# Optimization experiments

Hardware: AMD Instinct MI355X
Metric: run time of the kernel (lower is better)

The kernel has to match this reference:

```python
import jax, jax.numpy as jnp
import numpy as np
import itertools

N_SET = 4        # number of elements in the input set (input.size(-2))
IN_F = 2048      # in_features
OUT_F = 2048     # out_features
BOT = 512        # bottleneck_dim
B = 512          # batch size
NUM_NODES = 391
EMB_DIM = 300

# All nonempty subsets of range(N_SET), ordered by scale then lexicographic,
# exactly matching the torch loop over scales / itertools.combinations.
SUBSETS = [c for s in range(1, N_SET + 1) for c in itertools.combinations(range(N_SET), s)]

def _incl_matrix():
    # M[i, j] = 1 if SUBSETS[j] is a subset of SUBSETS[i].
    # This reproduces the dict-based scatter-sum: the aggregated output for rset
    # is the sum of raw Relation outputs over all nonempty k \subseteq rset.
    masks = [sum(1 << i for i in c) for c in SUBSETS]
    n = len(masks)
    M = np.zeros((n, n), dtype=np.float32)
    for i, mi in enumerate(masks):
        for j, mj in enumerate(masks):
            if (mj & mi) == mj:
                M[i, j] = 1.0
    return M

INCL = _incl_matrix()  # [15, 15]

def setup_inputs():
    key = jax.random.key(0)
    ks = jax.random.split(key, 16)
    inp = {"x": jax.random.normal(ks[0], (B, N_SET, IN_F), dtype=jnp.float32)}
    ki = 1
    for s in range(1, N_SET + 1):
        fan = s * IN_F
        inp[f"w1_s{s}"] = jax.random.normal(ks[ki], (BOT, fan), dtype=jnp.float32) / np.float32(np.sqrt(fan)); ki += 1
        inp[f"b1_s{s}"] = jnp.zeros((BOT,), dtype=jnp.float32)
        inp[f"w2_s{s}"] = jax.random.normal(ks[ki], (OUT_F, BOT), dtype=jnp.float32) / np.float32(np.sqrt(BOT)); ki += 1
        inp[f"b2_s{s}"] = jnp.zeros((OUT_F,), dtype=jnp.float32)
    inp["w_emb"] = jax.random.normal(ks[ki], (EMB_DIM, OUT_F), dtype=jnp.float32) / np.float32(np.sqrt(OUT_F)); ki += 1
    inp["b_emb"] = jnp.zeros((EMB_DIM,), dtype=jnp.float32)
    inp["w_node"] = jax.random.normal(ks[ki], (NUM_NODES, OUT_F), dtype=jnp.float32) / np.float32(np.sqrt(OUT_F)); ki += 1
    inp["b_node"] = jnp.zeros((NUM_NODES,), dtype=jnp.float32)
    return inp

def _base_forward(x, ws):
    # Batched per-scale Relation MLPs over all C(4,s) subsets at once.
    raws = []
    for s in range(1, N_SET + 1):
        idx = np.array(list(itertools.combinations(range(N_SET), s)))  # [C, s]
        g = x[:, idx, :]                                  # [B, C, s, F] gather
        h = g.reshape(g.shape[0], g.shape[1], s * IN_F)   # concat along subset
        w1, b1, w2, b2 = ws[s - 1]
        h = jax.nn.relu(h)
        h = jax.nn.relu(jnp.einsum('bcf,of->bco', h, w1) + b1)
        raws.append(jnp.einsum('bcd,od->bco', h, w2) + b2)  # [B, C, OUT_F]
    raw = jnp.concatenate(raws, axis=1)  # [B, 15, OUT_F]
    # Subset-inclusion scatter-sum, expressed as a dense 15x15 contraction.
    return jnp.einsum('ij,bjf->bif', jnp.asarray(INCL), raw)

def reference(x, w1_s1, b1_s1, w2_s1, b2_s1, w1_s2, b1_s2, w2_s2, b2_s2,
              w1_s3, b1_s3, w2_s3, b2_s3, w1_s4, b1_s4, w2_s4, b2_s4,
              w_emb, b_emb, w_node, b_node):
    ws = [(w1_s1, b1_s1, w2_s1, b2_s1), (w1_s2, b1_s2, w2_s2, b2_s2),
          (w1_s3, b1_s3, w2_s3, b2_s3), (w1_s4, b1_s4, w2_s4, b2_s4)]
    feats = _base_forward(x, ws)                              # [B, 15, OUT_F]
    embeddings = jnp.einsum('bnf,ef->bne', feats, w_emb) + b_emb  # [B, 15, 300]
    node_out = jnp.einsum('bnf,vf->bnv', feats, w_node) + b_node  # [B, 15, 391]
    return embeddings, jnp.swapaxes(node_out, -2, -1)             # [B, 391, 15]
```

## Files before the change

### kernel.cpp

```cpp
#include <hip/hip_runtime.h>
#include <stdint.h>

using bf16x8 = __attribute__((ext_vector_type(8))) short;
using f32x4  = __attribute__((ext_vector_type(4))) float;

#define DEVINL __device__ __forceinline__

DEVINL unsigned short f2bf(float f) {
  union { float f; unsigned u; } v; v.f = f;
  unsigned u = v.u;
  return (unsigned short)((u + 0x7FFFu + ((u >> 16) & 1u)) >> 16);
}
DEVINL float bf2f(unsigned short h) {
  union { unsigned u; float f; } v; v.u = ((unsigned)h) << 16;
  return v.f;
}

DEVINL void gload_lds16(const void* g, void* l) {
  __builtin_amdgcn_global_load_lds(
      (const __attribute__((address_space(1))) void*)g,
      (__attribute__((address_space(3))) void*)l, 16, 0, 0);
}

template<int OUT_BF16, int HAS_BIAS>
DEVINL void gemm_core(const unsigned short* __restrict__ A,
                      const unsigned short* __restrict__ B,
                      void* __restrict__ C,
                      const float* __restrict__ bias,
                      int K, int Cld, int arow0, int brow0, int crow0, int ccol0)
{
  __shared__ __align__(16) unsigned short As[3][256 * 64];
  __shared__ __align__(16) unsigned short Bs[3][128 * 64];

  const int t    = threadIdx.x;
  const int wave = t >> 6;
  const int lane = t & 63;
  const int wr   = (wave >> 1) << 6;
  const int wc   = (wave & 1) << 6;
  const int lrow = lane & 15;
  const int kg   = lane >> 4;

  f32x4 acc[4][4];
#pragma unroll
  for (int r = 0; r < 4; ++r)
#pragma unroll
    for (int q = 0; q < 4; ++q) acc[r][q] = (f32x4){0.f, 0.f, 0.f, 0.f};

  const int srow = t >> 3;
  const int scol = (((t & 7) ^ (srow & 7)) << 3);
  const unsigned short* aSrc = A + (size_t)(arow0 + srow) * K + scol;
  const unsigned short* bSrc = B + (size_t)(brow0 + srow) * K + scol;

  auto STAGE = [&](int slot, int kt) {
    const int k0 = kt << 6;
    char* aD = (char*)As[slot] + wave * 1024;
    char* bD = (char*)Bs[slot] + wave * 1024;
#pragma unroll
    for (int p = 0; p < 4; ++p)
      gload_lds16(aSrc + (size_t)(p * 64) * K + k0, aD + p * 8192);
#pragma unroll
    for (int p = 0; p < 2; ++p)
      gload_lds16(bSrc + (size_t)(p * 64) * K + k0, bD + p * 8192);
  };

  const int nt = K >> 6;
  STAGE(0, 0);
  STAGE(1, 1);

  const int rs = lrow & 7;
  const int cA0 = ((kg + 0) ^ rs) << 3;
  const int cA1 = ((kg + 4) ^ rs) << 3;

  int sl = 0;
  for (int kt = 0; kt < nt; ++kt) {
    const unsigned short* Ab = As[sl];
    const unsigned short* Bb = Bs[sl];
    if (kt + 2 < nt) {
      int s2 = sl + 2; if (s2 >= 3) s2 -= 3;
      STAGE(s2, kt + 2);
      asm volatile("s_waitcnt vmcnt(12)" ::: "memory");
    } else if (kt + 1 < nt) {
      asm volatile("s_waitcnt vmcnt(6)" ::: "memory");
    } else {
      asm volatile("s_waitcnt vmcnt(0)" ::: "memory");
    }
    __builtin_amdgcn_s_barrier();

    bf16x8 a0[4], b0[4], a1[4], b1[4];
#pragma unroll
    for (int r = 0; r < 4; ++r)
      a0[r] = *(const bf16x8*)&Ab[(wr + r * 16 + lrow) * 64 + cA0];
#pragma unroll
    for (int q = 0; q < 4; ++q)
      b0[q] = *(const bf16x8*)&Bb[(wc + q * 16 + lrow) * 64 + cA0];
    __builtin_amdgcn_s_setprio(1);
#pragma unroll
    for (int r = 0; r < 2; ++r)
#pragma unroll
      for (int q = 0; q < 4; ++q)
        acc[r][q] = __builtin_amdgcn_mfma_f32_16x16x32_bf16(a0[r], b0[q], acc[r][q], 0, 0, 0);
    __builtin_amdgcn_s_setprio(0);
    __builtin_amdgcn_s_barrier();
#pragma unroll
    for (int r = 0; r < 4; ++r)
      a1[r] = *(const bf16x8*)&Ab[(wr + r * 16 + lrow) * 64 + cA1];
#pragma unroll
    for (int q = 0; q < 4; ++q)
      b1[q] = *(const bf16x8*)&Bb[(wc + q * 16 + lrow) * 64 + cA1];
    __builtin_amdgcn_s_setprio(1);
#pragma unroll
    for (int r = 2; r < 4; ++r)
#pragma unroll
      for (int q = 0; q < 4; ++q)
        acc[r][q] = __builtin_amdgcn_mfma_f32_16x16x32_bf16(a0[r], b0[q], acc[r][q], 0, 0, 0);
    __builtin_amdgcn_s_setprio(0);
    __builtin_amdgcn_s_barrier();
    __builtin_amdgcn_s_setprio(1);
#pragma unroll
    for (int r = 0; r < 2; ++r)
#pragma unroll
      for (int q = 0; q < 4; ++q)
        acc[r][q] = __builtin_amdgcn_mfma_f32_16x16x32_bf16(a1[r], b1[q], acc[r][q], 0, 0, 0);
    __builtin_amdgcn_s_setprio(0);
    __builtin_amdgcn_s_barrier();
    __builtin_amdgcn_s_setprio(1);
#pragma unroll
    for (int r = 2; r < 4; ++r)
#pragma unroll
      for (int q = 0; q < 4; ++q)
        acc[r][q] = __builtin_amdgcn_mfma_f32_16x16x32_bf16(a1[r], b1[q], acc[r][q], 0, 0, 0);
    __builtin_amdgcn_s_setprio(0);
    __builtin_amdgcn_s_barrier();
    ++sl; if (sl == 3) sl = 0;
  }

#pragma unroll
  for (int r = 0; r < 4; ++r) {
#pragma unroll
    for (int q = 0; q < 4; ++q) {
      const int col = ccol0 + wc + q * 16 + lrow;
      const float bv = HAS_BIAS ? bias[col] : 0.f;
#pragma unroll
      for (int v = 0; v < 4; ++v) {
        const int row = crow0 + wr + r * 16 + (kg << 2) + v;
        const float val = acc[r][q][v] + bv;
        if (OUT_BF16)
          ((unsigned short*)C)[(size_t)row * Cld + col] = f2bf(val);
        else
          ((float*)C)[(size_t)row * Cld + col] = val;
      }
    }
  }
}

__global__ __launch_bounds__(512) void mega1_k(const unsigned short* __restrict__ xrb,
                                               const unsigned short* __restrict__ w1cat,
                                               const unsigned short* __restrict__ wen,
                                               const unsigned short* __restrict__ w2t,
                                               unsigned short* __restrict__ H0p,
                                               unsigned short* __restrict__ W2EN) {
  const int bid = blockIdx.x;
  if (bid < 160) {
    const int p = bid >> 3, q = bid & 7;
    const int rt = q >> 2, ct = q & 3;
    const int MM[20] = {0,1,2,3, 0,1,2, 1,2,3, 0,1, 1,2, 2,3, 0,1,2,3};
    const int JJ[20] = {0,0,0,0, 1,1,1, 2,2,2, 3,3, 4,4, 5,5, 6,7,8,9};
    gemm_core<1, 0>(xrb, w1cat, H0p, nullptr, 2048, 512,
                    MM[p] * 512 + rt * 256, JJ[p] * 512 + ct * 128,
                    p * 512 + rt * 256, ct * 128);
  } else {
    const int b2 = bid - 160;
    const int s = b2 / 12, r = b2 % 12;
    const int rt = r >> 2, ct = r & 3;
    gemm_core<1, 0>(wen, w2t, W2EN, nullptr, 2048, 512,
                    rt * 256, s * 512 + ct * 128,
                    s * 768 + rt * 256, ct * 128);
  }
}

__global__ __launch_bounds__(512) void gemmF_k(const unsigned short* __restrict__ h1,
                                               const unsigned short* __restrict__ W2EN,
                                               const float* __restrict__ ENb,
                                               float* __restrict__ EN0) {
  const int y = blockIdx.y;
  const int c = y >> 1;
  const int s = (c < 4) ? 1 : (c < 10) ? 2 : (c < 14) ? 3 : 4;
  gemm_core<0, 1>(h1, W2EN, EN0, ENb + (size_t)(s - 1) * 768, 512, 768,
                  y * 256, (s - 1) * 768 + blockIdx.x * 128,
                  y * 256, blockIdx.x * 128);
}

__global__ __launch_bounds__(256) void prep_all_k(const float* __restrict__ x,
                                                  const float* w11, const float* w12,
                                                  const float* w13, const float* w14,
                                                  const float* w21, const float* w22,
                                                  const float* w23, const float* w24,
                                                  const float* __restrict__ wemb,
                                                  const float* __restrict__ wnode,
                                                  const float* b21, const float* b22,
                                                  const float* b23, const float* b24,
                                                  unsigned short* __restrict__ xrb,
                                                  unsigned short* __restrict__ w1cat,
                                                  unsigned short* __restrict__ w2t,
                                                  unsigned short* __restrict__ wen,
                                                  float* __restrict__ ENb) {
  __shared__ float lds[64][65];
  __shared__ float red[4][4];
  const int bid = blockIdx.x;
  if (bid < 10240) {
    const int tid = bid * 256 + threadIdx.x;
    const int r = tid >> 9;
    const int k = (tid & 511) << 2;
    const int j = r >> 9, o = r & 511;
    const float* src; int s, tt;
    if (j == 0)      { src = w11; s = 1; tt = 0; }
    else if (j < 3)  { src = w12; s = 2; tt = j - 1; }
    else if (j < 6)  { src = w13; s = 3; tt = j - 3; }
    else             { src = w14; s = 4; tt = j - 6; }
    const float4 vv = *(const float4*)(src + (size_t)o * (s * 2048) + tt * 2048 + k);
    ushort4 ov;
    ov.x = f2bf(vv.x); ov.y = f2bf(vv.y); ov.z = f2bf(vv.z); ov.w = f2bf(vv.w);
    *(ushort4*)(w1cat + (size_t)r * 2048 + k) = ov;
  } else if (bid < 14336) {
    const int tid = (bid - 10240) * 256 + threadIdx.x;
    const int r = tid >> 9;
    const int k = (tid & 511) << 2;
    const int m = r >> 9, b = r & 511;
    const float4 vv = *(const float4*)(x + ((size_t)(b * 4 + m)) * 2048 + k);
    ushort4 o;
    o.x = f2bf(fmaxf(vv.x, 0.f)); o.y = f2bf(fmaxf(vv.y, 0.f));
    o.z = f2bf(fmaxf(vv.z, 0.f)); o.w = f2bf(fmaxf(vv.w, 0.f));
    *(ushort4*)(xrb + (size_t)r * 2048 + k) = o;
  } else if (bid < 15360) {
    const int idx = bid - 14336;
    const int s = idx >> 8, rem = idx & 255;
    const int rt = rem >> 3, ct = rem & 7;
    const float* src = (s == 0) ? w21 : (s == 1) ? w22 : (s == 2) ? w23 : w24;
    const int tr = threadIdx.x >> 4;
    const int tc = (threadIdx.x & 15) << 2;
#pragma unroll
    for (int i = 0; i < 4; ++i) {
      const float4 v = *(const float4*)(src + (size_t)(rt * 64 + tr + 16 * i) * 512 + ct * 64 + tc);
      lds[tr + 16 * i][tc + 0] = v.x; lds[tr + 16 * i][tc + 1] = v.y;
      lds[tr + 16 * i][tc + 2] = v.z; lds[tr + 16 * i][tc + 3] = v.w;
    }
    __syncthreads();
#pragma unroll
    for (int i = 0; i < 4; ++i) {
      ushort4 ov;
      ov.x = f2bf(lds[tc + 0][tr + 16 * i]); ov.y = f2bf(lds[tc + 1][tr + 16 * i]);
      ov.z = f2bf(lds[tc + 2][tr + 16 * i]); ov.w = f2bf(lds[tc + 3][tr + 16 * i]);
      *(ushort4*)(w2t + ((size_t)s * 512 + ct * 64 + tr + 16 * i) * 2048 + rt * 64 + tc) = ov;
    }
  } else if (bid < 16896) {
    const int tid = (bid - 15360) * 256 + threadIdx.x;
    const int r = tid >> 9;
    const int k = (tid & 511) << 2;
    float4 vv = make_float4(0.f, 0.f, 0.f, 0.f);
    if (r < 300)       vv = *(const float4*)(wemb + (size_t)r * 2048 + k);
    else if (r < 691)  vv = *(const float4*)(wnode + (size_t)(r - 300) * 2048 + k);
    ushort4 ov;
    ov.x = f2bf(vv.x); ov.y = f2bf(vv.y); ov.z = f2bf(vv.z); ov.w = f2bf(vv.w);
    *(ushort4*)(wen + (size_t)r * 2048 + k) = ov;
  } else {
    const int e = bid - 16896;
    const int t8 = threadIdx.x << 3;
    float a0 = 0.f, a1 = 0.f, a2 = 0.f, a3 = 0.f;
    if (e < 691) {
      const float* row = (e < 300) ? (wemb + (size_t)e * 2048)
                                   : (wnode + (size_t)(e - 300) * 2048);
      const float4 r0 = *(const float4*)(row + t8);
      const float4 r1 = *(const float4*)(row + t8 + 4);
      const float4 c10 = *(const float4*)(b21 + t8), c11 = *(const float4*)(b21 + t8 + 4);
      const float4 c20 = *(const float4*)(b22 + t8), c21 = *(const float4*)(b22 + t8 + 4);
      const float4 c30 = *(const float4*)(b23 + t8), c31 = *(const float4*)(b23 + t8 + 4);
      const float4 c40 = *(const float4*)(b24 + t8), c41 = *(const float4*)(b24 + t8 + 4);
      a0 = r0.x*c10.x + r0.y*c10.y + r0.z*c10.z + r0.w*c10.w
         + r1.x*c11.x + r1.y*c11.y + r1.z*c11.z + r1.w*c11.w;
      a1 = r0.x*c20.x + r0.y*c20.y + r0.z*c20.z + r0.w*c20.w
         + r1.x*c21.x + r1.y*c21.y + r1.z*c21.z + r1.w*c21.w;
      a2 = r0.x*c30.x + r0.y*c30.y + r0.z*c30.z + r0.w*c30.w
         + r1.x*c31.x + r1.y*c31.y + r1.z*c31.z + r1.w*c31.w;
      a3 = r0.x*c40.x + r0.y*c40.y + r0.z*c40.z + r0.w*c40.w
         + r1.x*c41.x + r1.y*c41.y + r1.z*c41.z + r1.w*c41.w;
    }
#pragma unroll
    for (int off = 32; off; off >>= 1) {
      a0 += __shfl_down(a0, off); a1 += __shfl_down(a1, off);
      a2 += __shfl_down(a2, off); a3 += __shfl_down(a3, off);
    }
    const int wv = threadIdx.x >> 6;
    if ((threadIdx.x & 63) == 0) {
      red[wv][0] = a0; red[wv][1] = a1; red[wv][2] = a2; red[wv][3] = a3;
    }
    __syncthreads();
    if (threadIdx.x < 4) {
      const float v = red[0][threadIdx.x] + red[1][threadIdx.x] +
                      red[2][threadIdx.x] + red[3][threadIdx.x];
      ENb[(size_t)threadIdx.x * 768 + e] = (e < 691) ? v : 0.f;
    }
  }
}

__global__ __launch_bounds__(128) void combine1_k(const unsigned short* __restrict__ H0p,
                                                  unsigned short* __restrict__ h1,
                                                  const float* __restrict__ b11,
                                                  const float* __restrict__ b12,
                                                  const float* __restrict__ b13,
                                                  const float* __restrict__ b14) {
  const int cb = blockIdx.x;
  const int c = cb >> 9, b = cb & 511;
  const int s = (c < 4) ? 1 : (c < 10) ? 2 : (c < 14) ? 3 : 4;
  const unsigned char P[15][4] = {
    {0,0,0,0},{1,0,0,0},{2,0,0,0},{3,0,0,0},
    {4,7,0,0},{4,8,0,0},{4,9,0,0},{5,8,0,0},{5,9,0,0},{6,9,0,0},
    {10,12,14,0},{10,12,15,0},{10,13,15,0},{11,13,15,0},
    {16,17,18,19}};
  const float* b1 = (s == 1) ? b11 : (s == 2) ? b12 : (s == 3) ? b13 : b14;
  const int o = threadIdx.x << 2;
  float4 a = *(const float4*)(b1 + o);
  for (int t = 0; t < s; ++t) {
    const int p = P[c][t];
    const ushort4 hv = *(const ushort4*)(H0p + ((size_t)(p * 512 + b)) * 512 + o);
    a.x += bf2f(hv.x); a.y += bf2f(hv.y); a.z += bf2f(hv.z); a.w += bf2f(hv.w);
  }
  ushort4 ov;
  ov.x = f2bf(fmaxf(a.x, 0.f)); ov.y = f2bf(fmaxf(a.y, 0.f));
  ov.z = f2bf(fmaxf(a.z, 0.f)); ov.w = f2bf(fmaxf(a.w, 0.f));
  *(ushort4*)(h1 + (size_t)cb * 512 + o) = ov;
}

__global__ __launch_bounds__(256) void combine2_k(const float* __restrict__ EN0,
                                                  const float* __restrict__ b_emb,
                                                  const float* __restrict__ b_node,
                                                  float* __restrict__ out0,
                                                  float* __restrict__ out1) {
  const int b   = blockIdx.x;
  const int col = blockIdx.y * 256 + threadIdx.x;
  if (col >= 691) return;
  float vals[15];
#pragma unroll
  for (int j = 0; j < 15; ++j)
    vals[j] = EN0[((size_t)(j * 512 + b)) * 768 + col];
  const int MSK[15] = {1,2,4,8,3,5,9,6,10,12,7,11,13,14,15};
  if (col < 300) {
    const float be = b_emb[col];
#pragma unroll
    for (int i = 0; i < 15; ++i) {
      float sum = be;
#pragma unroll
      for (int j = 0; j < 15; ++j)
        if ((MSK[j] & MSK[i]) == MSK[j]) sum += vals[j];
      out0[((size_t)b * 15 + i) * 300 + col] = sum;
    }
  } else {
    const int v = col - 300;
    const float bn = b_node[v];
#pragma unroll
    for (int i = 0; i < 15; ++i) {
      float sum = bn;
#pragma unroll
      for (int j = 0; j < 15; ++j)
        if ((MSK[j] & MSK[i]) == MSK[j]) sum += vals[j];
      out1[((size_t)b * 391 + v) * 15 + i] = sum;
    }
  }
}

extern "C" void kernel_launch(void* const* d_in, const int* in_sizes, int n_in,
                              void* d_out, int out_size, void* d_ws, size_t ws_size,
                              hipStream_t stream) {
  const float* x     = (const float*)d_in[0];
  const float* w11   = (const float*)d_in[1];
  const float* b11   = (const float*)d_in[2];
  const float* w21   = (const float*)d_in[3];
  const float* b21   = (const float*)d_in[4];
  const float* w12   = (const float*)d_in[5];
  const float* b12   = (const float*)d_in[6];
  const float* w22   = (const float*)d_in[7];
  const float* b22   = (const float*)d_in[8];
  const float* w13   = (const float*)d_in[9];
  const float* b13   = (const float*)d_in[10];
  const float* w23   = (const float*)d_in[11];
  const float* b23   = (const float*)d_in[12];
  const float* w14   = (const float*)d_in[13];
  const float* b14   = (const float*)d_in[14];
  const float* w24   = (const float*)d_in[15];
  const float* b24   = (const float*)d_in[16];
  const float* wemb  = (const float*)d_in[17];
  const float* bemb  = (const float*)d_in[18];
  const float* wnode = (const float*)d_in[19];
  const float* bnode = (const float*)d_in[20];

  char* ws = (char*)d_ws;
  unsigned short* xrb   = (unsigned short*)(ws + 0);
  unsigned short* w1cat = (unsigned short*)(ws + 8388608);
  unsigned short* w2t   = (unsigned short*)(ws + 29360128);
  unsigned short* wen   = (unsigned short*)(ws + 37748736);
  unsigned short* H0p   = (unsigned short*)(ws + 40894464);
  unsigned short* W2EN  = (unsigned short*)(ws + 51380224);
  float*          ENb   = (float*)(ws + 54525952);
  unsigned short* h1bf  = (unsigned short*)(ws + 54538240);
  float*          EN0   = (float*)(ws + 0);

  float* out0 = (float*)d_out;
  float* out1 = out0 + 2304000;

  prep_all_k<<<17664, 256, 0, stream>>>(x, w11, w12, w13, w14, w21, w22, w23, w24,
                                        wemb, wnode, b21, b22, b23, b24,
                                        xrb, w1cat, w2t, wen, ENb);
  mega1_k   <<<208, 512, 0, stream>>>(xrb, w1cat, wen, w2t, H0p, W2EN);
  combine1_k<<<7680, 128, 0, stream>>>(H0p, h1bf, b11, b12, b13, b14);
  gemmF_k   <<<dim3(6, 30), 512, 0, stream>>>(h1bf, W2EN, ENb, EN0);
  combine2_k<<<dim3(512, 3), 256, 0, stream>>>(EN0, bemb, bnode, out0, out1);
}
```

Before: 105.9 us.

## Split tile staging across two k-half phases and interleave with LDS reads and MFMA

The global-to-LDS prefetch of the next-next tile is split into two halves, each issued right after the LDS fragment reads of the matching k-half. The vmcnt wait moves to just before the second-half compute, and a prologue wait is added before the loop. The four quarter MFMA phases become two full 4x4 phases with fewer barriers and fewer live fragment registers. The aim is to spread memory issue and cut barrier overhead, at the cost of a tighter wait on the outstanding loads.

```diff
diff --git a/kernel.cpp b/kernel.cpp
--- a/kernel.cpp
+++ b/kernel.cpp
@@ -51,86 +51,81 @@
   const unsigned short* aSrc = A + (size_t)(arow0 + srow) * K + scol;
   const unsigned short* bSrc = B + (size_t)(brow0 + srow) * K + scol;
 
-  auto STAGE = [&](int slot, int kt) {
+  auto STAGE_S0 = [&](int slot, int kt) {
     const int k0 = kt << 6;
     char* aD = (char*)As[slot] + wave * 1024;
     char* bD = (char*)Bs[slot] + wave * 1024;
-#pragma unroll
-    for (int p = 0; p < 4; ++p)
-      gload_lds16(aSrc + (size_t)(p * 64) * K + k0, aD + p * 8192);
-#pragma unroll
-    for (int p = 0; p < 2; ++p)
-      gload_lds16(bSrc + (size_t)(p * 64) * K + k0, bD + p * 8192);
+    gload_lds16(aSrc + (size_t)0 * K + k0, aD);
+    gload_lds16(aSrc + (size_t)64 * K + k0, aD + 8192);
+    gload_lds16(bSrc + (size_t)0 * K + k0, bD);
   };
+  auto STAGE_S1 = [&](int slot, int kt) {
+    const int k0 = kt << 6;
+    char* aD = (char*)As[slot] + wave * 1024;
+    char* bD = (char*)Bs[slot] + wave * 1024;
+    gload_lds16(aSrc + (size_t)128 * K + k0, aD + 16384);
+    gload_lds16(aSrc + (size_t)192 * K + k0, aD + 24576);
+    gload_lds16(bSrc + (size_t)64 * K + k0, bD + 8192);
+  };
 
   const int nt = K >> 6;
-  STAGE(0, 0);
-  STAGE(1, 1);
+  STAGE_S0(0, 0); STAGE_S1(0, 0);
+  if (nt > 1) { STAGE_S0(1, 1); STAGE_S1(1, 1); }
 
   const int rs = lrow & 7;
   const int cA0 = ((kg + 0) ^ rs) << 3;
   const int cA1 = ((kg + 4) ^ rs) << 3;
+
+  if (nt > 1) { asm volatile("s_waitcnt vmcnt(6)" ::: "memory"); }
+  else        { asm volatile("s_waitcnt vmcnt(0)" ::: "memory"); }
+  __builtin_amdgcn_s_barrier();
 
   int sl = 0;
   for (int kt = 0; kt < nt; ++kt) {
     const unsigned short* Ab = As[sl];
     const unsigned short* Bb = Bs[sl];
-    if (kt + 2 < nt) {
-      int s2 = sl + 2; if (s2 >= 3) s2 -= 3;
-      STAGE(s2, kt + 2);
-      asm volatile("s_waitcnt vmcnt(12)" ::: "memory");
-    } else if (kt + 1 < nt) {
-      asm volatile("s_waitcnt vmcnt(6)" ::: "memory");
-    } else {
-      asm volatile("s_waitcnt vmcnt(0)" ::: "memory");
-    }
+    int s2 = sl + 2; if (s2 >= 3) s2 -= 3;
+
+    bf16x8 af[4], bq[4];
+#pragma unroll
+    for (int r = 0; r < 4; ++r)
+      af[r] = *(const bf16x8*)&Ab[(wr + r * 16 + lrow) * 64 + cA0];
+#pragma unroll
+    for (int q = 0; q < 4; ++q)
+      bq[q] = *(const bf16x8*)&Bb[(wc + q * 16 + lrow) * 64 + cA0];
+    if (kt + 2 < nt) STAGE_S0(s2, kt + 2);
     __builtin_amdgcn_s_barrier();
-
-    bf16x8 a0[4], b0[4], a1[4], b1[4];
+    __builtin_amdgcn_s_setprio(1);
 #pragma unroll
     for (int r = 0; r < 4; ++r)
-      a0[r] = *(const bf16x8*)&Ab[(wr + r * 16 + lrow) * 64 + cA0];
-#pragma unroll
-    for (int q = 0; q < 4; ++q)
-      b0[q] = *(const bf16x8*)&Bb[(wc + q * 16 + lrow) * 64 + cA0];
-    __builtin_amdgcn_s_setprio(1);
-#pragma unroll
-    for (int r = 0; r < 2; ++r)
 #pragma unroll
       for (int q = 0; q < 4; ++q)
-        acc[r][q] = __builtin_amdgcn_mfma_f32_16x16x32_bf16(a0[r], b0[q], acc[r][q], 0, 0, 0);
+        acc[r][q] = __builtin_amdgcn_mfma_f32_16x16x32_bf16(af[r], bq[q], acc[r][q], 0, 0, 0);
     __builtin_amdgcn_s_setprio(0);
     __builtin_amdgcn_s_barrier();
+
 #pragma unroll
     for (int r = 0; r < 4; ++r)
-      a1[r] = *(const bf16x8*)&Ab[(wr + r * 16 + lrow) * 64 + cA1];
+      af[r] = *(const bf16x8*)&Ab[(wr + r * 16 + lrow) * 64 + cA1];
 #pragma unroll
     for (int q = 0; q < 4; ++q)
-      b1[q] = *(const bf16x8*)&Bb[(wc + q * 16 + lrow) * 64 + cA1];
+      bq[q] = *(const bf16x8*)&Bb[(wc + q * 16 + lrow) * 64 + cA1];
+    if (kt + 2 < nt) {
+      STAGE_S1(s2, kt + 2);
+      asm volatile("s_waitcnt vmcnt(6)" ::: "memory");
+    } else if (kt + 1 < nt) {
+      asm volatile("s_waitcnt vmcnt(0)" ::: "memory");
+    }
+    __builtin_amdgcn_s_barrier();
     __builtin_amdgcn_s_setprio(1);
 #pragma unroll
-    for (int r = 2; r < 4; ++r)
+    for (int r = 0; r < 4; ++r)
 #pragma unroll
       for (int q = 0; q < 4; ++q)
-        acc[r][q] = __builtin_amdgcn_mfma_f32_16x16x32_bf16(a0[r], b0[q], acc[r][q], 0, 0, 0);
+        acc[r][q] = __builtin_amdgcn_mfma_f32_16x16x32_bf16(af[r], bq[q], acc[r][q], 0, 0, 0);
     __builtin_amdgcn_s_setprio(0);
     __builtin_amdgcn_s_barrier();
-    __builtin_amdgcn_s_setprio(1);
-#pragma unroll
-    for (int r = 0; r < 2; ++r)
-#pragma unroll
-      for (int q = 0; q < 4; ++q)
-        acc[r][q] = __builtin_amdgcn_mfma_f32_16x16x32_bf16(a1[r], b1[q], acc[r][q], 0, 0, 0);
-    __builtin_amdgcn_s_setprio(0);
-    __builtin_amdgcn_s_barrier();
-    __builtin_amdgcn_s_setprio(1);
-#pragma unroll
-    for (int r = 2; r < 4; ++r)
-#pragma unroll
-      for (int q = 0; q < 4; ++q)
-        acc[r][q] = __builtin_amdgcn_mfma_f32_16x16x32_bf16(a1[r], b1[q], acc[r][q], 0, 0, 0);
-    __builtin_amdgcn_s_setprio(0);
-    __builtin_amdgcn_s_barrier();
+
     ++sl; if (sl == 3) sl = 0;
   }
 
```

Result: faster. 92.46 us (-12.7%).
